# Kernel tuning notes

Measured on AMD Instinct MI355X. Metric: run time of the kernel, lower is better.

Reference implementation:

```python
import jax, jax.numpy as jnp
import numpy as np

NUM_EXPERTS = 8
DIM = 2048
BATCH = 8192


def setup_inputs() -> dict:
    key = jax.random.key(0)
    k_x, k_ids, k_w, k_b = jax.random.split(key, 4)
    x = jax.random.normal(k_x, (BATCH, DIM), dtype=jnp.float32)
    cam_pred_ids = jax.random.randint(k_ids, (BATCH,), 0, NUM_EXPERTS, dtype=jnp.int64)
    # torch nn.Linear default init: U(-1/sqrt(in), 1/sqrt(in)); W is [out, in]
    bound = 1.0 / np.sqrt(DIM)
    W = jax.random.uniform(k_w, (NUM_EXPERTS, DIM, DIM), dtype=jnp.float32,
                           minval=-bound, maxval=bound)
    b = jax.random.uniform(k_b, (NUM_EXPERTS, DIM), dtype=jnp.float32,
                           minval=-bound, maxval=bound)
    return {"x": x, "cam_pred_ids": cam_pred_ids, "W": W, "b": b}


def reference(x, cam_pred_ids, W, b):
    # Per-sample expert routing: out[i] = x[i] + relu(x[i] @ W[e].T + b[e]),
    # where e = cam_pred_ids[i]. Vectorized as 8 full-batch GEMMs with masked
    # combine (fixed small expert count -> Python loop is structural, not data).
    h = jnp.zeros_like(x)
    for e in range(NUM_EXPERTS):
        he = jax.nn.relu(x @ W[e].T + b[e])          # [B, D]
        mask = (cam_pred_ids == e)[:, None]
        h = h + jnp.where(mask, he, jnp.zeros((), dtype=x.dtype))
    return x + h
```

## Files before the change

### kernel.cpp

```cpp
#include <hip/hip_runtime.h>
#include <hip/hip_bf16.h>
#include <stdint.h>

#define BATCH 8192
#define DIM   2048
#define NEXP  8
#define BM    128
#define BN    128
#define BK    32
#define NITER (DIM / BK)
#define MAX_TILES 72
#define NBLK  (DIM / BN)
#define NPAD  1024
#define NCVT  16384

typedef __bf16 bf16x8 __attribute__((ext_vector_type(8)));
typedef float  f32x4  __attribute__((ext_vector_type(4)));

#define XG_BYTE_OFF 40960ull
#define WB_BYTE_OFF 37789696ull
#define WS_NEED     104898560ull

#define AS1(p) ((const __attribute__((address_space(1))) void*)(p))
#define AS3(p) ((__attribute__((address_space(3))) void*)(p))

__device__ __forceinline__ unsigned f2bf2(float lo, float hi) {
    unsigned ul = __float_as_uint(lo), uh = __float_as_uint(hi);
    ul = (ul + 0x7FFFu + ((ul >> 16) & 1u)) >> 16;
    uh = (uh + 0x7FFFu + ((uh >> 16) & 1u)) >> 16;
    return (uh << 16) | ul;
}

__global__ void k_plan(const int* __restrict__ ids, int* __restrict__ ws) {
    __shared__ int sc[NEXP];
    int t = threadIdx.x;
    if (t < NEXP) sc[t] = 0;
    __syncthreads();
    for (int i = t; i < BATCH; i += 256) atomicAdd(&sc[ids[i]], 1);
    __syncthreads();
    if (t == 0) {
        int pos = 0, mt = 0;
        for (int e = 0; e < NEXP; e++) {
            int c = sc[e];
            ws[e]      = c;
            ws[16 + e] = 0;
            ws[32 + e] = pos;
            int ntl = (c + BM - 1) / BM;
            for (int tt = 0; tt < ntl; tt++) {
                ws[64  + mt] = e;
                ws[160 + mt] = pos + tt * BM;
                int v = c - tt * BM;
                ws[256 + mt] = v < BM ? v : BM;
                mt++;
            }
            pos += ntl * BM;
        }
        ws[48] = mt;
    }
}

__global__ void k_prep(const float* __restrict__ x, const int* __restrict__ ids,
                       int* __restrict__ ws, unsigned short* __restrict__ xg,
                       int* __restrict__ rowmap,
                       const float4* __restrict__ W, uint4* __restrict__ Wb) {
    int b = blockIdx.x;
    if (b >= BATCH + NPAD) {
        size_t o = (size_t)(b - (BATCH + NPAD)) * 256 + threadIdx.x;
        float4 a = W[o * 2], c = W[o * 2 + 1];
        uint4 v;
        v.x = f2bf2(a.x, a.y);  v.y = f2bf2(a.z, a.w);
        v.z = f2bf2(c.x, c.y);  v.w = f2bf2(c.z, c.w);
        Wb[o] = v;
        return;
    }
    if (b >= BATCH) {
        int p = b - BATCH;
        int row = -1;
        for (int e = 0; e < NEXP; e++) {
            int c = ws[e];
            int pe = ((c + BM - 1) & ~(BM - 1)) - c;
            if (p < pe) { row = ws[32 + e] + c + p; break; }
            p -= pe;
        }
        if (row < 0) return;
        uint4* o = (uint4*)(xg + (size_t)row * DIM);
        uint4 z = make_uint4(0, 0, 0, 0);
        for (int t = threadIdx.x; t < DIM / 8; t += 256) o[t] = z;
        return;
    }
    __shared__ int spos;
    if (threadIdx.x == 0) {
        int e = ids[b];
        int p = ws[32 + e] + atomicAdd(&ws[16 + e], 1);
        spos = p;
        rowmap[p] = b;
    }
    __syncthreads();
    int pos = spos;
    const float4* xr = (const float4*)(x + (size_t)b * DIM);
    uint4* o = (uint4*)(xg + (size_t)pos * DIM);
    int t = threadIdx.x;
    float4 a = xr[t * 2], b4 = xr[t * 2 + 1];
    uint4 v;
    v.x = f2bf2(a.x, a.y);   v.y = f2bf2(a.z, a.w);
    v.z = f2bf2(b4.x, b4.y); v.w = f2bf2(b4.z, b4.w);
    o[t] = v;
}

__launch_bounds__(256)
__global__ void k_gemm(const unsigned short* __restrict__ xg,
                       const unsigned short* __restrict__ Wb,
                       const float* __restrict__ bias,
                       const int* __restrict__ ws, const int* __restrict__ rowmap,
                       float* __restrict__ out) {
    int bid = blockIdx.x;
    int g = bid >> 3, r = bid & 7;
    int nb = g & 15;
    int mt = ((g >> 4) << 3) + r;
    if (mt >= ws[48]) return;
    int e     = ws[64  + mt];
    int pos0  = ws[160 + mt];
    int valid = ws[256 + mt];
    int n0 = nb * BN;

    __shared__ unsigned short lds[3][8192];

    int tid = threadIdx.x;
    int w = tid >> 6, l = tid & 63;
    int lane15 = l & 15, quad = l >> 4;
    int wave_m = (w >> 1) * 64, wave_n = (w & 1) * 64;

    const unsigned short* Abase = xg + (size_t)pos0 * DIM;
    const unsigned short* Bbase = Wb + (size_t)e * DIM * DIM + (size_t)n0 * DIM;

    int srcOff[2];
#pragma unroll
    for (int j = 0; j < 2; j++) {
        int c = w * 128 + j * 64 + l;
        int row = c >> 2, pos = c & 3;
        int q = pos ^ ((row >> 1) & 3);
        srcOff[j] = row * DIM + q * 8;
    }

    int swz = (quad ^ ((lane15 >> 1) & 3)) * 8;
    int afOff[4], bfOff[4];
#pragma unroll
    for (int mi = 0; mi < 4; mi++)
        afOff[mi] = (wave_m + mi * 16 + lane15) * BK + swz;
#pragma unroll
    for (int ni = 0; ni < 4; ni++)
        bfOff[ni] = 4096 + (wave_n + ni * 16 + lane15) * BK + swz;

    f32x4 acc[4][4];
#pragma unroll
    for (int i = 0; i < 4; i++)
#pragma unroll
        for (int j = 0; j < 4; j++) acc[i][j] = (f32x4){0.f, 0.f, 0.f, 0.f};

#define ISSUE(buf, k0)                                                          \
    do {                                                                        \
        _Pragma("unroll")                                                       \
        for (int j = 0; j < 2; j++) {                                           \
            __builtin_amdgcn_global_load_lds(                                   \
                AS1(Abase + (k0) + srcOff[j]),                                  \
                AS3(&lds[buf][w * 1024 + j * 512]), 16, 0, 0);                  \
            __builtin_amdgcn_global_load_lds(                                   \
                AS1(Bbase + (k0) + srcOff[j]),                                  \
                AS3(&lds[buf][4096 + w * 1024 + j * 512]), 16, 0, 0);           \
        }                                                                       \
    } while (0)

    ISSUE(0, 0);
    ISSUE(1, BK);
    int cur = 0;
    for (int i = 0; i < NITER; ++i) {
        if (i + 1 < NITER) asm volatile("s_waitcnt vmcnt(4)" ::: "memory");
        else               asm volatile("s_waitcnt vmcnt(0)" ::: "memory");
        __builtin_amdgcn_s_barrier();
        asm volatile("" ::: "memory");
        if (i + 2 < NITER) {
            int nb3 = cur + 2; if (nb3 >= 3) nb3 -= 3;
            ISSUE(nb3, (i + 2) * BK);
        }
        bf16x8 af[4], bf[4];
#pragma unroll
        for (int mi = 0; mi < 4; mi++)
            af[mi] = *(const bf16x8*)(&lds[cur][afOff[mi]]);
#pragma unroll
        for (int ni = 0; ni < 4; ni++)
            bf[ni] = *(const bf16x8*)(&lds[cur][bfOff[ni]]);
#pragma unroll
        for (int mi = 0; mi < 4; mi++)
#pragma unroll
            for (int ni = 0; ni < 4; ni++)
                acc[mi][ni] = __builtin_amdgcn_mfma_f32_16x16x32_bf16(
                    af[mi], bf[ni], acc[mi][ni], 0, 0, 0);
        if (++cur == 3) cur = 0;
    }
#undef ISSUE

    float bv[4];
#pragma unroll
    for (int ni = 0; ni < 4; ni++)
        bv[ni] = bias[(size_t)e * DIM + n0 + wave_n + ni * 16 + lane15];
#pragma unroll
    for (int mi = 0; mi < 4; mi++) {
#pragma unroll
        for (int r4 = 0; r4 < 4; r4++) {
            int rl = wave_m + mi * 16 + quad * 4 + r4;
            if (rl < valid) {
                int orig = rowmap[pos0 + rl];
                const unsigned short* xrow = xg + (size_t)(pos0 + rl) * DIM + n0;
                float* orow = out + (size_t)orig * DIM + n0;
#pragma unroll
                for (int ni = 0; ni < 4; ni++) {
                    int col = wave_n + ni * 16 + lane15;
                    float xv = __uint_as_float((unsigned)xrow[col] << 16);
                    float v = acc[mi][ni][r4] + bv[ni];
                    v = v > 0.f ? v : 0.f;
                    orow[col] = xv + v;
                }
            }
        }
    }
}

__global__ void k_naive(const float* __restrict__ x, const int* __restrict__ ids,
                        const float* __restrict__ W, const float* __restrict__ b,
                        float* __restrict__ out) {
    __shared__ float lx[DIM];
    int i = blockIdx.x;
    for (int t = threadIdx.x; t < DIM; t += blockDim.x) lx[t] = x[(size_t)i * DIM + t];
    __syncthreads();
    int e = ids[i];
    const float* We = W + (size_t)e * DIM * DIM;
    for (int n = threadIdx.x; n < DIM; n += blockDim.x) {
        const float* wr = We + (size_t)n * DIM;
        float acc = 0.f;
        for (int k = 0; k < DIM; k += 4) {
            float4 w4 = *(const float4*)(wr + k);
            acc += lx[k] * w4.x + lx[k + 1] * w4.y + lx[k + 2] * w4.z + lx[k + 3] * w4.w;
        }
        float v = acc + b[(size_t)e * DIM + n];
        v = v > 0.f ? v : 0.f;
        out[(size_t)i * DIM + n] = lx[n] + v;
    }
}

extern "C" void kernel_launch(void* const* d_in, const int* in_sizes, int n_in,
                              void* d_out, int out_size, void* d_ws, size_t ws_size,
                              hipStream_t stream) {
    const float* x   = (const float*)d_in[0];
    const int*   ids = (const int*)d_in[1];
    const float* W   = (const float*)d_in[2];
    const float* b   = (const float*)d_in[3];
    float* out = (float*)d_out;

    if (ws_size < WS_NEED) {
        k_naive<<<BATCH, 256, 0, stream>>>(x, ids, W, b, out);
        return;
    }

    char* wsb = (char*)d_ws;
    int*  wsi = (int*)wsb;
    unsigned short* xg = (unsigned short*)(wsb + XG_BYTE_OFF);
    unsigned short* Wb = (unsigned short*)(wsb + WB_BYTE_OFF);
    int* rowmap = wsi + 512;

    k_plan<<<1, 256, 0, stream>>>(ids, wsi);
    k_prep<<<BATCH + NPAD + NCVT, 256, 0, stream>>>(x, ids, wsi, xg, rowmap,
                                                    (const float4*)W, (uint4*)Wb);
    k_gemm<<<NBLK * MAX_TILES, 256, 0, stream>>>(xg, Wb, b, wsi, rowmap, out);
}
```

Before: 468.2 us.

## Build rowmap via counting sort in plan, simplify prep, double-buffer GEMM

k_plan now computes per-thread expert histograms and prefix offsets in a single block, then writes the full gather rowmap with -1 marking padding rows. This removes the per-row atomics and the separate padding-block search from k_prep. k_prep becomes one block per gathered row, and each weight-conversion block now handles four chunks, so far fewer blocks are launched. The GEMM drops from a 3-stage LDS ring with a partial vmcnt wait to 2-stage double buffering with a full __syncthreads. That cuts LDS use to 32KB, which may raise occupancy, but it reduces how much global-load latency is hidden behind MFMA work.

```diff
diff --git a/kernel.cpp b/kernel.cpp
--- a/kernel.cpp
+++ b/kernel.cpp
@@ -11,8 +11,8 @@
 #define NITER (DIM / BK)
 #define MAX_TILES 72
 #define NBLK  (DIM / BN)
-#define NPAD  1024
-#define NCVT  16384
+#define NROWS 9216
+#define NCVTB 4096
 
 typedef __bf16 bf16x8 __attribute__((ext_vector_type(8)));
 typedef float  f32x4  __attribute__((ext_vector_type(4)));
@@ -31,19 +31,33 @@
     return (uh << 16) | ul;
 }
 
-__global__ void k_plan(const int* __restrict__ ids, int* __restrict__ ws) {
-    __shared__ int sc[NEXP];
+__global__ void k_plan(const int* __restrict__ ids, int* __restrict__ ws,
+                       int* __restrict__ rowmap) {
+    __shared__ int sc[256 * NEXP];
+    __shared__ int seg[NEXP];
+    __shared__ int tot[NEXP];
     int t = threadIdx.x;
-    if (t < NEXP) sc[t] = 0;
-    __syncthreads();
-    for (int i = t; i < BATCH; i += 256) atomicAdd(&sc[ids[i]], 1);
+#pragma unroll
+    for (int e = 0; e < NEXP; e++) sc[t * NEXP + e] = 0;
+    int base = t * 32;
+    for (int i = 0; i < 32; i++) sc[t * NEXP + ids[base + i]]++;
+    __syncthreads();
+    if (t < NEXP) {
+        int run = 0;
+        for (int j = 0; j < 256; j++) {
+            int v = sc[j * NEXP + t];
+            sc[j * NEXP + t] = run;
+            run += v;
+        }
+        tot[t] = run;
+    }
     __syncthreads();
     if (t == 0) {
         int pos = 0, mt = 0;
         for (int e = 0; e < NEXP; e++) {
-            int c = sc[e];
+            int c = tot[e];
+            seg[e]     = pos;
             ws[e]      = c;
-            ws[16 + e] = 0;
             ws[32 + e] = pos;
             int ntl = (c + BM - 1) / BM;
             for (int tt = 0; tt < ntl; tt++) {
@@ -56,50 +70,44 @@
             pos += ntl * BM;
         }
         ws[48] = mt;
-    }
-}
-
-__global__ void k_prep(const float* __restrict__ x, const int* __restrict__ ids,
-                       int* __restrict__ ws, unsigned short* __restrict__ xg,
-                       int* __restrict__ rowmap,
+        ws[49] = pos;
+    }
+    __syncthreads();
+    for (int i = t; i < NROWS; i += 256) rowmap[i] = -1;
+    __syncthreads();
+    for (int i = 0; i < 32; i++) {
+        int e = ids[base + i];
+        int p = seg[e] + sc[t * NEXP + e]++;
+        rowmap[p] = base + i;
+    }
+}
+
+__global__ void k_prep(const float* __restrict__ x,
+                       const int* __restrict__ rowmap,
+                       unsigned short* __restrict__ xg,
                        const float4* __restrict__ W, uint4* __restrict__ Wb) {
     int b = blockIdx.x;
-    if (b >= BATCH + NPAD) {
-        size_t o = (size_t)(b - (BATCH + NPAD)) * 256 + threadIdx.x;
-        float4 a = W[o * 2], c = W[o * 2 + 1];
-        uint4 v;
-        v.x = f2bf2(a.x, a.y);  v.y = f2bf2(a.z, a.w);
-        v.z = f2bf2(c.x, c.y);  v.w = f2bf2(c.z, c.w);
-        Wb[o] = v;
+    int t = threadIdx.x;
+    if (b >= NROWS) {
+        size_t base = (size_t)(b - NROWS) * 1024;
+#pragma unroll
+        for (int j = 0; j < 4; j++) {
+            size_t o = base + (size_t)j * 256 + t;
+            float4 a = W[o * 2], c = W[o * 2 + 1];
+            uint4 v;
+            v.x = f2bf2(a.x, a.y);  v.y = f2bf2(a.z, a.w);
+            v.z = f2bf2(c.x, c.y);  v.w = f2bf2(c.z, c.w);
+            Wb[o] = v;
+        }
         return;
     }
-    if (b >= BATCH) {
-        int p = b - BATCH;
-        int row = -1;
-        for (int e = 0; e < NEXP; e++) {
-            int c = ws[e];
-            int pe = ((c + BM - 1) & ~(BM - 1)) - c;
-            if (p < pe) { row = ws[32 + e] + c + p; break; }
-            p -= pe;
-        }
-        if (row < 0) return;
-        uint4* o = (uint4*)(xg + (size_t)row * DIM);
-        uint4 z = make_uint4(0, 0, 0, 0);
-        for (int t = threadIdx.x; t < DIM / 8; t += 256) o[t] = z;
+    int orig = rowmap[b];
+    uint4* o = (uint4*)(xg + (size_t)b * DIM);
+    if (orig < 0) {
+        o[t] = make_uint4(0, 0, 0, 0);
         return;
     }
-    __shared__ int spos;
-    if (threadIdx.x == 0) {
-        int e = ids[b];
-        int p = ws[32 + e] + atomicAdd(&ws[16 + e], 1);
-        spos = p;
-        rowmap[p] = b;
-    }
-    __syncthreads();
-    int pos = spos;
-    const float4* xr = (const float4*)(x + (size_t)b * DIM);
-    uint4* o = (uint4*)(xg + (size_t)pos * DIM);
-    int t = threadIdx.x;
+    const float4* xr = (const float4*)(x + (size_t)orig * DIM);
     float4 a = xr[t * 2], b4 = xr[t * 2 + 1];
     uint4 v;
     v.x = f2bf2(a.x, a.y);   v.y = f2bf2(a.z, a.w);
@@ -123,7 +131,7 @@
     int valid = ws[256 + mt];
     int n0 = nb * BN;
 
-    __shared__ unsigned short lds[3][8192];
+    __shared__ unsigned short lds[2][8192];
 
     int tid = threadIdx.x;
     int w = tid >> 6, l = tid & 63;
@@ -171,16 +179,12 @@
     } while (0)
 
     ISSUE(0, 0);
-    ISSUE(1, BK);
     int cur = 0;
     for (int i = 0; i < NITER; ++i) {
-        if (i + 1 < NITER) asm volatile("s_waitcnt vmcnt(4)" ::: "memory");
-        else               asm volatile("s_waitcnt vmcnt(0)" ::: "memory");
-        __builtin_amdgcn_s_barrier();
-        asm volatile("" ::: "memory");
-        if (i + 2 < NITER) {
-            int nb3 = cur + 2; if (nb3 >= 3) nb3 -= 3;
-            ISSUE(nb3, (i + 2) * BK);
+        __syncthreads();
+        if (i + 1 < NITER) {
+            int k0n = (i + 1) * BK;
+            ISSUE(cur ^ 1, k0n);
         }
         bf16x8 af[4], bf[4];
 #pragma unroll
@@ -195,7 +199,7 @@
             for (int ni = 0; ni < 4; ni++)
                 acc[mi][ni] = __builtin_amdgcn_mfma_f32_16x16x32_bf16(
                     af[mi], bf[ni], acc[mi][ni], 0, 0, 0);
-        if (++cur == 3) cur = 0;
+        cur ^= 1;
     }
 #undef ISSUE
 
@@ -267,8 +271,8 @@
     unsigned short* Wb = (unsigned short*)(wsb + WB_BYTE_OFF);
     int* rowmap = wsi + 512;
 
-    k_plan<<<1, 256, 0, stream>>>(ids, wsi);
-    k_prep<<<BATCH + NPAD + NCVT, 256, 0, stream>>>(x, ids, wsi, xg, rowmap,
-                                                    (const float4*)W, (uint4*)Wb);
+    k_plan<<<1, 256, 0, stream>>>(ids, wsi, rowmap);
+    k_prep<<<NROWS + NCVTB, 256, 0, stream>>>(x, rowmap, xg,
+                                              (const float4*)W, (uint4*)Wb);
     k_gemm<<<NBLK * MAX_TILES, 256, 0, stream>>>(xg, Wb, b, wsi, rowmap, out);
 }
```

Result: faster. 403.0 us (-13.9%).
